# Optimization experiments

Measured on AMD Instinct MI355X. Metric: run time of the kernel, lower is better.

The kernel has to match this reference:

```python
import jax, jax.numpy as jnp
import numpy as np

H = 16          # num heads
KV_LORA = 512   # absorbed v dim
ROPE = 64       # qk_rope_head_dim
QK = KV_LORA + ROPE  # 576 absorbed qk dim
EPS = 1e-6


def rms_norm(x, w):
    xf = x.astype(jnp.float32)
    var = jnp.mean(xf * xf, axis=-1, keepdims=True)
    return (w * (xf * jax.lax.rsqrt(var + EPS))).astype(x.dtype)


def rotate_half(x):
    x1, x2 = jnp.split(x, 2, axis=-1)
    return jnp.concatenate([-x2, x1], axis=-1)


def apply_rope(x, cos, sin):
    # x: [B,S,H,ROPE]; cos/sin: [B,S,ROPE] -> broadcast over head dim
    c = cos[:, :, None, :]
    s = sin[:, :, None, :]
    return x * c + rotate_half(x) * s


def setup_inputs() -> dict:
    key = jax.random.key(0)
    ks = jax.random.split(key, 10)
    B, S, D = 1, 2048, 2048
    Q_LORA, TOPK = 1536, 512
    hidden_states = jax.random.normal(ks[0], (B, S, D), jnp.float32)
    cos = jax.random.uniform(ks[1], (B, S, ROPE), jnp.float32)
    sin = jax.random.uniform(ks[2], (B, S, ROPE), jnp.float32)
    topk = jax.random.randint(ks[3], (B, S, TOPK), 0, S)
    # guarantee the diagonal is selected so no softmax row is fully masked
    topk = topk.at[:, :, 0].set(jnp.arange(S)[None, :])
    sc = lambda f_in: 1.0 / np.sqrt(f_in)
    w_q_a = jax.random.normal(ks[4], (Q_LORA, D), jnp.float32) * sc(D)
    w_q_a_ln = jnp.ones((Q_LORA,), jnp.float32)
    w_q_b = jax.random.normal(ks[5], (H * QK, Q_LORA), jnp.float32) * sc(Q_LORA)
    w_kv_a = jax.random.normal(ks[6], (QK, D), jnp.float32) * sc(D)
    w_kv_a_ln = jnp.ones((KV_LORA,), jnp.float32)
    w_o = jax.random.normal(ks[7], (D, H * KV_LORA), jnp.float32) * sc(H * KV_LORA)
    return {"hidden_states": hidden_states, "cos": cos, "sin": sin,
            "topk_indices": topk, "w_q_a": w_q_a, "w_q_a_ln": w_q_a_ln,
            "w_q_b": w_q_b, "w_kv_a": w_kv_a, "w_kv_a_ln": w_kv_a_ln, "w_o": w_o}


def reference(hidden_states, cos, sin, topk_indices, w_q_a, w_q_a_ln, w_q_b,
              w_kv_a, w_kv_a_ln, w_o):
    B, S, D = hidden_states.shape
    # ---- Q path (low-rank + absorbed kv_b nope) ----
    q_resid = rms_norm(hidden_states @ w_q_a.T, w_q_a_ln)        # [B,S,1536]
    q = (q_resid @ w_q_b.T).reshape(B, S, H, QK)                  # [B,S,H,576]
    q_nope, q_pe = q[..., :KV_LORA], q[..., KV_LORA:]
    q_pe = apply_rope(q_pe, cos, sin)
    q = jnp.concatenate([q_nope, q_pe], axis=-1)                  # [B,S,H,576]
    # ---- shared latent KV (MQA over 576-d cache entry) ----
    ckv = hidden_states @ w_kv_a.T                                # [B,S,576]
    k_c = rms_norm(ckv[..., :KV_LORA], w_kv_a_ln)
    k_pe = apply_rope(ckv[..., KV_LORA:][:, :, None, :], cos, sin)[:, :, 0, :]
    kv = jnp.concatenate([k_c, k_pe], axis=-1)                    # [B,S,576]
    v = kv[..., :KV_LORA]                                         # [B,S,512]
    # ---- DSA sparse + causal mask ----
    allowed = jnp.zeros((B, S, S), bool)
    bi = jnp.arange(B)[:, None, None]
    si = jnp.arange(S)[None, :, None]
    allowed = allowed.at[bi, si, topk_indices].set(True)          # scatter topk
    causal = jnp.tril(jnp.ones((S, S), bool))[None]
    mask = jnp.where(allowed & causal, 0.0, -jnp.inf)[:, None]    # [B,1,S,S]
    # ---- attention ----
    scaling = QK ** (-0.5)
    scores = jnp.einsum('bshd,btd->bhst', q, kv) * scaling + mask
    probs = jax.nn.softmax(scores.astype(jnp.float32), axis=-1).astype(q.dtype)
    attn = jnp.einsum('bhst,btd->bshd', probs, v)                 # [B,S,H,512]
    out = attn.reshape(B, S, H * KV_LORA) @ w_o.T                 # [B,S,D]
    return out
```

## Files before the change

kernel.cpp:

```cpp
#include <hip/hip_runtime.h>
#include <hip/hip_bf16.h>
#include <cstdint>

#define S_LEN   2048
#define DMODEL  2048
#define HHEADS  16
#define KVLORA  512
#define ROPE_D  64
#define QKD     576
#define QLORA   1536
#define TOPK    512
#define HQK     (HHEADS * QKD)
#define HKV     (HHEADS * KVLORA)
#define NKV_PAD 640

typedef __attribute__((ext_vector_type(4))) float f4v;
typedef __attribute__((ext_vector_type(8))) short short8;
typedef __attribute__((ext_vector_type(2))) unsigned int u32x2;
typedef __attribute__((ext_vector_type(4))) unsigned int u32x4;

__device__ __forceinline__ ushort f2bf(float f) {
  uint32_t u = __float_as_uint(f);
  uint32_t r = (u + 0x7fffu + ((u >> 16) & 1u)) >> 16;
  return (ushort)r;
}
__device__ __forceinline__ float bf2f(ushort u) {
  return __uint_as_float(((uint32_t)u) << 16);
}

__device__ __forceinline__ void gload_lds16(const ushort* g, ushort* l) {
  __builtin_amdgcn_global_load_lds(
      (const __attribute__((address_space(1))) unsigned int*)(uintptr_t)g,
      (__attribute__((address_space(3))) unsigned int*)(uintptr_t)l,
      16, 0, 0);
}

__global__ __launch_bounds__(256)
void gemm_bf16_nt(const ushort* __restrict__ A, const ushort* __restrict__ B,
                  float* __restrict__ C, int M, int N, int K) {
  __shared__ ushort As[128 * 32];
  __shared__ ushort Bs[128 * 32];
  const int tid = threadIdx.x;
  const int lane = tid & 63;
  const int w = tid >> 6;
  const int wr = w >> 1, wc = w & 1;
  const int bm = blockIdx.y * 128, bn = blockIdx.x * 128;

  f4v acc[4][4];
#pragma unroll
  for (int m = 0; m < 4; ++m)
#pragma unroll
    for (int n = 0; n < 4; ++n) acc[m][n] = (f4v){0.f, 0.f, 0.f, 0.f};

  const int ar0 = w * 32;
  const int srow = lane >> 2;
  const int scol = (lane & 3) * 8;
  const int koff = (lane >> 4) * 8;
  const int fr = lane & 15;

  for (int k0 = 0; k0 < K; k0 += 32) {
    __syncthreads();
    gload_lds16(A + (size_t)(bm + ar0 + srow) * K + k0 + scol, &As[ar0 * 32]);
    gload_lds16(A + (size_t)(bm + ar0 + 16 + srow) * K + k0 + scol, &As[(ar0 + 16) * 32]);
    gload_lds16(B + (size_t)(bn + ar0 + srow) * K + k0 + scol, &Bs[ar0 * 32]);
    gload_lds16(B + (size_t)(bn + ar0 + 16 + srow) * K + k0 + scol, &Bs[(ar0 + 16) * 32]);
    __syncthreads();

    short8 a[4], b[4];
#pragma unroll
    for (int m = 0; m < 4; ++m)
      a[m] = *(const short8*)&As[(wr * 64 + m * 16 + fr) * 32 + koff];
#pragma unroll
    for (int n = 0; n < 4; ++n)
      b[n] = *(const short8*)&Bs[(wc * 64 + n * 16 + fr) * 32 + koff];
#pragma unroll
    for (int m = 0; m < 4; ++m)
#pragma unroll
      for (int n = 0; n < 4; ++n)
        acc[m][n] = __builtin_amdgcn_mfma_f32_16x16x32_bf16(a[m], b[n], acc[m][n], 0, 0, 0);
  }

  const int crow0 = bm + wr * 64 + (lane >> 4) * 4;
  const int ccol0 = bn + wc * 64 + (lane & 15);
#pragma unroll
  for (int m = 0; m < 4; ++m)
#pragma unroll
    for (int n = 0; n < 4; ++n)
#pragma unroll
      for (int r = 0; r < 4; ++r)
        C[(size_t)(crow0 + m * 16 + r) * N + ccol0 + n * 16] = acc[m][n][r];
}

__global__ __launch_bounds__(256)
void gemm_bf16_nt_bf16out(const ushort* __restrict__ A, const ushort* __restrict__ B,
                          ushort* __restrict__ C, int M, int N, int K) {
  __shared__ ushort As[128 * 32];
  __shared__ ushort Bs[128 * 32];
  const int tid = threadIdx.x;
  const int lane = tid & 63;
  const int w = tid >> 6;
  const int wr = w >> 1, wc = w & 1;
  const int bm = blockIdx.y * 128, bn = blockIdx.x * 128;

  f4v acc[4][4];
#pragma unroll
  for (int m = 0; m < 4; ++m)
#pragma unroll
    for (int n = 0; n < 4; ++n) acc[m][n] = (f4v){0.f, 0.f, 0.f, 0.f};

  const int ar0 = w * 32;
  const int srow = lane >> 2;
  const int scol = (lane & 3) * 8;
  const int koff = (lane >> 4) * 8;
  const int fr = lane & 15;

  for (int k0 = 0; k0 < K; k0 += 32) {
    __syncthreads();
    gload_lds16(A + (size_t)(bm + ar0 + srow) * K + k0 + scol, &As[ar0 * 32]);
    gload_lds16(A + (size_t)(bm + ar0 + 16 + srow) * K + k0 + scol, &As[(ar0 + 16) * 32]);
    gload_lds16(B + (size_t)(bn + ar0 + srow) * K + k0 + scol, &Bs[ar0 * 32]);
    gload_lds16(B + (size_t)(bn + ar0 + 16 + srow) * K + k0 + scol, &Bs[(ar0 + 16) * 32]);
    __syncthreads();

    short8 a[4], b[4];
#pragma unroll
    for (int m = 0; m < 4; ++m)
      a[m] = *(const short8*)&As[(wr * 64 + m * 16 + fr) * 32 + koff];
#pragma unroll
    for (int n = 0; n < 4; ++n)
      b[n] = *(const short8*)&Bs[(wc * 64 + n * 16 + fr) * 32 + koff];
#pragma unroll
    for (int m = 0; m < 4; ++m)
#pragma unroll
      for (int n = 0; n < 4; ++n)
        acc[m][n] = __builtin_amdgcn_mfma_f32_16x16x32_bf16(a[m], b[n], acc[m][n], 0, 0, 0);
  }

  const int crow0 = bm + wr * 64 + (lane >> 4) * 4;
  const int ccol0 = bn + wc * 64 + (lane & 15);
#pragma unroll
  for (int m = 0; m < 4; ++m)
#pragma unroll
    for (int n = 0; n < 4; ++n)
#pragma unroll
      for (int r = 0; r < 4; ++r)
        C[(size_t)(crow0 + m * 16 + r) * N + ccol0 + n * 16] = f2bf(acc[m][n][r]);
}

__global__ __launch_bounds__(256)
void cast_bf16(const float* __restrict__ in, ushort* __restrict__ out, int n8) {
  int i = blockIdx.x * 256 + threadIdx.x;
  if (i >= n8) return;
  float4 v0 = ((const float4*)in)[i * 2];
  float4 v1 = ((const float4*)in)[i * 2 + 1];
  short8 r;
  r[0] = f2bf(v0.x); r[1] = f2bf(v0.y); r[2] = f2bf(v0.z); r[3] = f2bf(v0.w);
  r[4] = f2bf(v1.x); r[5] = f2bf(v1.y); r[6] = f2bf(v1.z); r[7] = f2bf(v1.w);
  ((short8*)out)[i] = r;
}

__global__ __launch_bounds__(256)
void cast_pad_bf16(const float* __restrict__ in, ushort* __restrict__ out,
                   int rows_in, int cols, int n8) {
  int i = blockIdx.x * 256 + threadIdx.x;
  if (i >= n8) return;
  int row = (i * 8) / cols;
  short8 r = (short8){0, 0, 0, 0, 0, 0, 0, 0};
  if (row < rows_in) {
    float4 v0 = ((const float4*)in)[i * 2];
    float4 v1 = ((const float4*)in)[i * 2 + 1];
    r[0] = f2bf(v0.x); r[1] = f2bf(v0.y); r[2] = f2bf(v0.z); r[3] = f2bf(v0.w);
    r[4] = f2bf(v1.x); r[5] = f2bf(v1.y); r[6] = f2bf(v1.z); r[7] = f2bf(v1.w);
  }
  ((short8*)out)[i] = r;
}

__global__ __launch_bounds__(256)
void rmsnorm_bf16(const float* __restrict__ x, const float* __restrict__ w,
                  ushort* __restrict__ y, int n, float inv_n) {
  const int row = blockIdx.x;
  const float* p = x + (size_t)row * n;
  ushort* yp = y + (size_t)row * n;
  const int tid = threadIdx.x;
  const int n4 = n / 4;
  float ss = 0.f;
  for (int i = tid; i < n4; i += 256) {
    float4 v = ((const float4*)p)[i];
    ss += v.x * v.x + v.y * v.y + v.z * v.z + v.w * v.w;
  }
#pragma unroll
  for (int d = 32; d >= 1; d >>= 1) ss += __shfl_xor(ss, d);
  __shared__ float wsum[4];
  if ((tid & 63) == 0) wsum[tid >> 6] = ss;
  __syncthreads();
  float tot = wsum[0] + wsum[1] + wsum[2] + wsum[3];
  float inv = rsqrtf(tot * inv_n + 1e-6f);
  for (int i = tid; i < n4; i += 256) {
    float4 v = ((const float4*)p)[i];
    float4 g = ((const float4*)w)[i];
    ushort4 o;
    o.x = f2bf(g.x * v.x * inv); o.y = f2bf(g.y * v.y * inv);
    o.z = f2bf(g.z * v.z * inv); o.w = f2bf(g.w * v.w * inv);
    ((ushort4*)yp)[i] = o;
  }
}

__global__ __launch_bounds__(256)
void rope_scale(ushort* __restrict__ q, const float* __restrict__ cs,
                const float* __restrict__ sn) {
  const int s = blockIdx.x;
  const int tid = threadIdx.x;
  __shared__ float c_s[64], s_s[64];
  if (tid < 64) { c_s[tid] = cs[s * 64 + tid]; s_s[tid] = sn[s * 64 + tid]; }
  __syncthreads();
  const float SC = 0.041666666666666664f;
  ushort* qrow = q + (size_t)s * HQK;
  for (int i = tid; i < 1024; i += 256) {
    int hh = i >> 6, c = i & 63;
    ushort* p = qrow + hh * QKD + c * 8;
    short8 v = *(short8*)p;
#pragma unroll
    for (int e = 0; e < 8; ++e) v[e] = (short)f2bf(bf2f((ushort)v[e]) * SC);
    *(short8*)p = v;
  }
  for (int i = tid; i < HHEADS * 32; i += 256) {
    int hh = i >> 5, r = i & 31;
    ushort* bp = qrow + hh * QKD + KVLORA;
    float x1 = bf2f(bp[r]), x2 = bf2f(bp[r + 32]);
    bp[r]      = f2bf((x1 * c_s[r] - x2 * s_s[r]) * SC);
    bp[r + 32] = f2bf((x2 * c_s[r + 32] + x1 * s_s[r + 32]) * SC);
  }
}

__global__ __launch_bounds__(64)
void kv_build_bf(const float* __restrict__ ckv, const float* __restrict__ lnw,
                 const float* __restrict__ cs, const float* __restrict__ sn,
                 ushort* __restrict__ kvbf) {
  const int s = blockIdx.x;
  const int lane = threadIdx.x;
  const float* row = ckv + (size_t)s * NKV_PAD;
  float4 a = ((const float4*)row)[lane * 2];
  float4 b = ((const float4*)row)[lane * 2 + 1];
  float ss = a.x * a.x + a.y * a.y + a.z * a.z + a.w * a.w +
             b.x * b.x + b.y * b.y + b.z * b.z + b.w * b.w;
#pragma unroll
  for (int d = 32; d >= 1; d >>= 1) ss += __shfl_xor(ss, d);
  float inv = rsqrtf(ss * (1.f / KVLORA) + 1e-6f);
  float4 wa = ((const float4*)lnw)[lane * 2];
  float4 wb = ((const float4*)lnw)[lane * 2 + 1];
  ushort* orow = kvbf + (size_t)s * QKD;
  short8 o;
  o[0] = f2bf(a.x * wa.x * inv); o[1] = f2bf(a.y * wa.y * inv);
  o[2] = f2bf(a.z * wa.z * inv); o[3] = f2bf(a.w * wa.w * inv);
  o[4] = f2bf(b.x * wb.x * inv); o[5] = f2bf(b.y * wb.y * inv);
  o[6] = f2bf(b.z * wb.z * inv); o[7] = f2bf(b.w * wb.w * inv);
  *(short8*)(orow + lane * 8) = o;
  float x = row[KVLORA + lane];
  int partner = (lane < 32) ? lane + 32 : lane - 32;
  float other = row[KVLORA + partner];
  float rot = (lane < 32) ? -other : other;
  orow[KVLORA + lane] = f2bf(x * cs[s * 64 + lane] + rot * sn[s * 64 + lane]);
}

__global__ __launch_bounds__(256)
void attn_mfma(const ushort* __restrict__ qbf, const ushort* __restrict__ kvbf,
               const int* __restrict__ topk, ushort* __restrict__ attn_out) {
  const int s = blockIdx.x;
  const int tid = threadIdx.x;
  const int lane = tid & 63;
  const int w = tid >> 6;
  const int g = lane >> 4;
  const int h = lane & 15;

  __shared__ unsigned int msk[64];
  __shared__ int list[544];
  __shared__ int nk_s;
  __shared__ float wred[4][16];
  __shared__ float denom_lds[16];
  __shared__ ushort P_lds[16][520];
  __shared__ ushort VT[32 * 32 * 16];

  if (tid < 64) msk[tid] = 0u;
  {
    uint* pz = (uint*)&P_lds[0][0];
    for (int i = tid; i < 16 * 260; i += 256) pz[i] = 0u;
  }
  __syncthreads();
  for (int i = tid; i < TOPK; i += 256) {
    int t = topk[(size_t)s * TOPK + i];
    if (t <= s) atomicOr(&msk[t >> 5], 1u << (t & 31));
  }
  __syncthreads();

  if (w == 0) {
    unsigned int b = msk[lane];
    int cnt = __popc(b);
    int incl = cnt;
#pragma unroll
    for (int d = 1; d < 64; d <<= 1) {
      int o = __shfl_up(incl, d);
      if (lane >= d) incl += o;
    }
    if (lane == 63) nk_s = incl;
    int pos = incl - cnt;
    while (b) {
      int bit = __ffs(b) - 1;
      list[pos++] = (lane << 5) + bit;
      b &= b - 1;
    }
    int nkv = __shfl(incl, 63);
    for (int i = nkv + lane; i < 544; i += 64) list[i] = s;
  }

  short8 qf[18];
  const ushort* qrow = qbf + (size_t)s * HQK + h * QKD;
#pragma unroll
  for (int kk = 0; kk < 18; ++kk)
    qf[kk] = *(const short8*)(qrow + kk * 32 + g * 8);

  __syncthreads();
  const int nk = nk_s;
  const int nt16 = (nk + 15) >> 4;
  const int nkc = (nk + 31) >> 5;

  float sreg[8][4];
#pragma unroll
  for (int t2 = 0; t2 < 4; ++t2) {
    const int mtA = w + 8 * t2;
    const int mtB = mtA + 4;
    if (mtA >= nt16) break;
    const bool hasB = (mtB < nt16);
    const ushort* rA = kvbf + (size_t)list[mtA * 16 + h] * QKD;
    const ushort* rB = kvbf + (size_t)list[(hasB ? mtB : mtA) * 16 + h] * QKD;
    f4v aA = (f4v){0.f, 0.f, 0.f, 0.f};
    f4v aB = (f4v){0.f, 0.f, 0.f, 0.f};
#pragma unroll 6
    for (int kk = 0; kk < 18; ++kk) {
      short8 kfA = *(const short8*)(rA + kk * 32 + g * 8);
      short8 kfB = *(const short8*)(rB + kk * 32 + g * 8);
      aA = __builtin_amdgcn_mfma_f32_16x16x32_bf16(kfA, qf[kk], aA, 0, 0, 0);
      aB = __builtin_amdgcn_mfma_f32_16x16x32_bf16(kfB, qf[kk], aB, 0, 0, 0);
    }
#pragma unroll
    for (int r = 0; r < 4; ++r) {
      sreg[2 * t2][r] = aA[r];
      sreg[2 * t2 + 1][r] = aB[r];
    }
  }

  float mloc = -3e38f;
#pragma unroll
  for (int ti = 0; ti < 8; ++ti) {
    int keyb = 16 * (w + 4 * ti) + 4 * g;
#pragma unroll
    for (int r = 0; r < 4; ++r) {
      if (keyb + r >= nk) sreg[ti][r] = -3e38f;
      mloc = fmaxf(mloc, sreg[ti][r]);
    }
  }
  mloc = fmaxf(mloc, __shfl_xor(mloc, 16));
  mloc = fmaxf(mloc, __shfl_xor(mloc, 32));
  if (g == 0) wred[w][h] = mloc;
  __syncthreads();
  float mg = fmaxf(fmaxf(wred[0][h], wred[1][h]), fmaxf(wred[2][h], wred[3][h]));
  float psum = 0.f;
#pragma unroll
  for (int ti = 0; ti < 8; ++ti)
#pragma unroll
    for (int r = 0; r < 4; ++r) {
      float p = __expf(sreg[ti][r] - mg);
      sreg[ti][r] = p;
      psum += p;
    }
  psum += __shfl_xor(psum, 16);
  psum += __shfl_xor(psum, 32);
  __syncthreads();
  if (g == 0) wred[w][h] = psum;
  __syncthreads();
  float tot = wred[0][h] + wred[1][h] + wred[2][h] + wred[3][h];
  if (w == 0 && g == 0) denom_lds[h] = 1.0f / tot;

#pragma unroll
  for (int ti = 0; ti < 8; ++ti) {
    int mt = w + 4 * ti;
    if (mt >= nt16) break;
    uint lo = (uint)f2bf(sreg[ti][0]) | ((uint)f2bf(sreg[ti][1]) << 16);
    uint hi = (uint)f2bf(sreg[ti][2]) | ((uint)f2bf(sreg[ti][3]) << 16);
    uint* dst = (uint*)&P_lds[h][16 * mt + 4 * g];
    dst[0] = lo;
    dst[1] = hi;
  }

  f4v oacc[8];
#pragma unroll
  for (int j = 0; j < 8; ++j) oacc[j] = (f4v){0.f, 0.f, 0.f, 0.f};

  const uint vt_base = (uint)(size_t)(&VT[0]);

  for (int kc = 0; kc < nkc; ++kc) {
    __syncthreads();
#pragma unroll
    for (int ii = 0; ii < 8; ++ii) {
      int i = tid + ii * 256;
      int key = i >> 6, c = i & 63;
      const ushort* src = kvbf + (size_t)list[kc * 32 + key] * QKD + c * 8;
      short8 v = *(const short8*)src;
      *(short8*)&VT[(((c >> 1) * 32) + key) * 16 + (c & 1) * 8] = v;
    }
    __syncthreads();

    short8 pa = *(const short8*)&P_lds[h][kc * 32 + g * 8];
    u32x2 b0[8], b1[8];
#pragma unroll
    for (int j = 0; j < 8; ++j) {
      uint addr = vt_base + (uint)((w * 8 + j) * 1024 + g * 256 + h * 8);
      asm volatile("ds_read_b64_tr_b16 %0, %1 offset:0" : "=v"(b0[j]) : "v"(addr));
      asm volatile("ds_read_b64_tr_b16 %0, %1 offset:128" : "=v"(b1[j]) : "v"(addr));
    }
    asm volatile("s_waitcnt lgkmcnt(0)" ::: "memory");
    __builtin_amdgcn_sched_barrier(0);
#pragma unroll
    for (int j = 0; j < 8; ++j) {
      union { u32x4 u; short8 sv; } bb;
      bb.u = (u32x4){b0[j][0], b0[j][1], b1[j][0], b1[j][1]};
      oacc[j] = __builtin_amdgcn_mfma_f32_16x16x32_bf16(pa, bb.sv, oacc[j], 0, 0, 0);
    }
  }

  float rd[4];
#pragma unroll
  for (int r = 0; r < 4; ++r) rd[r] = denom_lds[4 * g + r];
  ushort* orow = attn_out + (size_t)s * HKV;
#pragma unroll
  for (int j = 0; j < 8; ++j) {
    int dcol = (w * 8 + j) * 16 + h;
#pragma unroll
    for (int r = 0; r < 4; ++r)
      orow[(size_t)(4 * g + r) * KVLORA + dcol] = f2bf(oacc[j][r] * rd[r]);
  }
}

extern "C" void kernel_launch(void* const* d_in, const int* in_sizes, int n_in,
                              void* d_out, int out_size, void* d_ws, size_t ws_size,
                              hipStream_t stream) {
  const float* hidden   = (const float*)d_in[0];
  const float* cosp     = (const float*)d_in[1];
  const float* sinp     = (const float*)d_in[2];
  const int*   topk     = (const int*)d_in[3];
  const float* w_q_a    = (const float*)d_in[4];
  const float* w_q_a_ln = (const float*)d_in[5];
  const float* w_q_b    = (const float*)d_in[6];
  const float* w_kv_a   = (const float*)d_in[7];
  const float* w_kv_ln  = (const float*)d_in[8];
  const float* w_o      = (const float*)d_in[9];
  float* out = (float*)d_out;

  char* base = (char*)d_ws;
  ushort* hid_bf  = (ushort*)(base + 0);
  ushort* wqa_bf  = (ushort*)(base + 8388608);
  float*  qa      = (float*) (base + 14680064);
  ushort* qa_bf   = (ushort*)(base + 27262976);
  ushort* attn_bf = (ushort*)(base + 0);
  ushort* wqb_bf  = (ushort*)(base + 33554432);
  ushort* wkv_bf  = (ushort*)(base + 61865984);
  ushort* wo_bf   = (ushort*)(base + 64487424);
  ushort* qbuf_bf = (ushort*)(base + 98041856);
  float*  ckv     = (float*) (base + 135790592);
  ushort* kv_bf   = (ushort*)(base + 141033472);

  cast_bf16<<<(S_LEN * DMODEL / 8 + 255) / 256, 256, 0, stream>>>(hidden, hid_bf, S_LEN * DMODEL / 8);
  cast_bf16<<<(QLORA * DMODEL / 8 + 255) / 256, 256, 0, stream>>>(w_q_a, wqa_bf, QLORA * DMODEL / 8);
  cast_bf16<<<(HQK * QLORA / 8 + 255) / 256, 256, 0, stream>>>(w_q_b, wqb_bf, HQK * QLORA / 8);
  cast_pad_bf16<<<(NKV_PAD * DMODEL / 8 + 255) / 256, 256, 0, stream>>>(w_kv_a, wkv_bf, QKD, DMODEL, NKV_PAD * DMODEL / 8);
  cast_bf16<<<(DMODEL * HKV / 8 + 255) / 256, 256, 0, stream>>>(w_o, wo_bf, DMODEL * HKV / 8);

  gemm_bf16_nt<<<dim3(QLORA / 128, S_LEN / 128), 256, 0, stream>>>(
      hid_bf, wqa_bf, qa, S_LEN, QLORA, DMODEL);
  rmsnorm_bf16<<<S_LEN, 256, 0, stream>>>(qa, w_q_a_ln, qa_bf, QLORA, 1.f / QLORA);

  gemm_bf16_nt_bf16out<<<dim3(HQK / 128, S_LEN / 128), 256, 0, stream>>>(
      qa_bf, wqb_bf, qbuf_bf, S_LEN, HQK, QLORA);
  rope_scale<<<S_LEN, 256, 0, stream>>>(qbuf_bf, cosp, sinp);

  gemm_bf16_nt<<<dim3(NKV_PAD / 128, S_LEN / 128), 256, 0, stream>>>(
      hid_bf, wkv_bf, ckv, S_LEN, NKV_PAD, DMODEL);
  kv_build_bf<<<S_LEN, 64, 0, stream>>>(ckv, w_kv_ln, cosp, sinp, kv_bf);

  attn_mfma<<<S_LEN, 256, 0, stream>>>(qbuf_bf, kv_bf, topk, attn_bf);

  gemm_bf16_nt<<<dim3(DMODEL / 128, S_LEN / 128), 256, 0, stream>>>(
      attn_bf, wo_bf, out, S_LEN, DMODEL, HKV);
}
```

Before: 755.8 us.

## Template GEMM with double-buffered LDS staging and per-call tile shapes

Replaces the two GEMM kernels with one templated kernel. It double-buffers the LDS tiles so the global_load_lds for the next K-slice is issued before the MFMAs of the current one, leaving one barrier per iteration instead of two. Each projection also gets its own tile shape: 64x128 for the q_a and output GEMMs and 64x64 for the small kv_a GEMM, which raises the workgroup count on the 256-CU device. The costs are doubled LDS footprint and smaller tiles that reuse less data. The async LDS loads are not explicitly waited on before the barrier, so correctness depends on the compiler inserting vmcnt waits.

```diff
diff --git a/kernel.cpp b/kernel.cpp
--- a/kernel.cpp
+++ b/kernel.cpp
@@ -35,116 +35,83 @@
       16, 0, 0);
 }
 
-__global__ __launch_bounds__(256)
-void gemm_bf16_nt(const ushort* __restrict__ A, const ushort* __restrict__ B,
-                  float* __restrict__ C, int M, int N, int K) {
-  __shared__ ushort As[128 * 32];
-  __shared__ ushort Bs[128 * 32];
+template<int BM, int BN, int WGM, int WGN, bool BF16OUT>
+__global__ __launch_bounds__(256)
+void gemm_nt_t(const ushort* __restrict__ A, const ushort* __restrict__ B,
+               void* __restrict__ Cv, int M, int N, int K) {
+  constexpr int MR = BM / (WGM * 16);
+  constexpr int NR = BN / (WGN * 16);
+  __shared__ ushort As[2][BM * 32];
+  __shared__ ushort Bs[2][BN * 32];
   const int tid = threadIdx.x;
   const int lane = tid & 63;
   const int w = tid >> 6;
-  const int wr = w >> 1, wc = w & 1;
-  const int bm = blockIdx.y * 128, bn = blockIdx.x * 128;
-
-  f4v acc[4][4];
-#pragma unroll
-  for (int m = 0; m < 4; ++m)
-#pragma unroll
-    for (int n = 0; n < 4; ++n) acc[m][n] = (f4v){0.f, 0.f, 0.f, 0.f};
-
-  const int ar0 = w * 32;
-  const int srow = lane >> 2;
+  const int wr = w / WGN, wc = w % WGN;
+  const int bm = blockIdx.y * BM, bn = blockIdx.x * BN;
+  const int srow16 = w * 16 + (lane >> 2);
   const int scol = (lane & 3) * 8;
   const int koff = (lane >> 4) * 8;
   const int fr = lane & 15;
 
-  for (int k0 = 0; k0 < K; k0 += 32) {
+  f4v acc[MR][NR];
+#pragma unroll
+  for (int m = 0; m < MR; ++m)
+#pragma unroll
+    for (int n = 0; n < NR; ++n) acc[m][n] = (f4v){0.f, 0.f, 0.f, 0.f};
+
+  auto STAGE = [&](int buf, int k0) {
+#pragma unroll
+    for (int r0 = 0; r0 < BM; r0 += 64)
+      gload_lds16(A + (size_t)(bm + r0 + srow16) * K + k0 + scol,
+                  &As[buf][(r0 + w * 16) * 32]);
+#pragma unroll
+    for (int r0 = 0; r0 < BN; r0 += 64)
+      gload_lds16(B + (size_t)(bn + r0 + srow16) * K + k0 + scol,
+                  &Bs[buf][(r0 + w * 16) * 32]);
+  };
+
+  const int nt = K / 32;
+  int cur = 0;
+  STAGE(0, 0);
+  for (int t = 0; t < nt; ++t) {
     __syncthreads();
-    gload_lds16(A + (size_t)(bm + ar0 + srow) * K + k0 + scol, &As[ar0 * 32]);
-    gload_lds16(A + (size_t)(bm + ar0 + 16 + srow) * K + k0 + scol, &As[(ar0 + 16) * 32]);
-    gload_lds16(B + (size_t)(bn + ar0 + srow) * K + k0 + scol, &Bs[ar0 * 32]);
-    gload_lds16(B + (size_t)(bn + ar0 + 16 + srow) * K + k0 + scol, &Bs[(ar0 + 16) * 32]);
-    __syncthreads();
-
-    short8 a[4], b[4];
-#pragma unroll
-    for (int m = 0; m < 4; ++m)
-      a[m] = *(const short8*)&As[(wr * 64 + m * 16 + fr) * 32 + koff];
-#pragma unroll
-    for (int n = 0; n < 4; ++n)
-      b[n] = *(const short8*)&Bs[(wc * 64 + n * 16 + fr) * 32 + koff];
-#pragma unroll
-    for (int m = 0; m < 4; ++m)
-#pragma unroll
-      for (int n = 0; n < 4; ++n)
+    if (t + 1 < nt) STAGE(cur ^ 1, (t + 1) * 32);
+    short8 a[MR], b[NR];
+#pragma unroll
+    for (int m = 0; m < MR; ++m)
+      a[m] = *(const short8*)&As[cur][(wr * MR * 16 + m * 16 + fr) * 32 + koff];
+#pragma unroll
+    for (int n = 0; n < NR; ++n)
+      b[n] = *(const short8*)&Bs[cur][(wc * NR * 16 + n * 16 + fr) * 32 + koff];
+#pragma unroll
+    for (int m = 0; m < MR; ++m)
+#pragma unroll
+      for (int n = 0; n < NR; ++n)
         acc[m][n] = __builtin_amdgcn_mfma_f32_16x16x32_bf16(a[m], b[n], acc[m][n], 0, 0, 0);
-  }
-
-  const int crow0 = bm + wr * 64 + (lane >> 4) * 4;
-  const int ccol0 = bn + wc * 64 + (lane & 15);
-#pragma unroll
-  for (int m = 0; m < 4; ++m)
-#pragma unroll
-    for (int n = 0; n < 4; ++n)
-#pragma unroll
-      for (int r = 0; r < 4; ++r)
-        C[(size_t)(crow0 + m * 16 + r) * N + ccol0 + n * 16] = acc[m][n][r];
-}
-
-__global__ __launch_bounds__(256)
-void gemm_bf16_nt_bf16out(const ushort* __restrict__ A, const ushort* __restrict__ B,
-                          ushort* __restrict__ C, int M, int N, int K) {
-  __shared__ ushort As[128 * 32];
-  __shared__ ushort Bs[128 * 32];
-  const int tid = threadIdx.x;
-  const int lane = tid & 63;
-  const int w = tid >> 6;
-  const int wr = w >> 1, wc = w & 1;
-  const int bm = blockIdx.y * 128, bn = blockIdx.x * 128;
-
-  f4v acc[4][4];
-#pragma unroll
-  for (int m = 0; m < 4; ++m)
-#pragma unroll
-    for (int n = 0; n < 4; ++n) acc[m][n] = (f4v){0.f, 0.f, 0.f, 0.f};
-
-  const int ar0 = w * 32;
-  const int srow = lane >> 2;
-  const int scol = (lane & 3) * 8;
-  const int koff = (lane >> 4) * 8;
-  const int fr = lane & 15;
-
-  for (int k0 = 0; k0 < K; k0 += 32) {
-    __syncthreads();
-    gload_lds16(A + (size_t)(bm + ar0 + srow) * K + k0 + scol, &As[ar0 * 32]);
-    gload_lds16(A + (size_t)(bm + ar0 + 16 + srow) * K + k0 + scol, &As[(ar0 + 16) * 32]);
-    gload_lds16(B + (size_t)(bn + ar0 + srow) * K + k0 + scol, &Bs[ar0 * 32]);
-    gload_lds16(B + (size_t)(bn + ar0 + 16 + srow) * K + k0 + scol, &Bs[(ar0 + 16) * 32]);
-    __syncthreads();
-
-    short8 a[4], b[4];
-#pragma unroll
-    for (int m = 0; m < 4; ++m)
-      a[m] = *(const short8*)&As[(wr * 64 + m * 16 + fr) * 32 + koff];
-#pragma unroll
-    for (int n = 0; n < 4; ++n)
-      b[n] = *(const short8*)&Bs[(wc * 64 + n * 16 + fr) * 32 + koff];
-#pragma unroll
-    for (int m = 0; m < 4; ++m)
-#pragma unroll
-      for (int n = 0; n < 4; ++n)
-        acc[m][n] = __builtin_amdgcn_mfma_f32_16x16x32_bf16(a[m], b[n], acc[m][n], 0, 0, 0);
-  }
-
-  const int crow0 = bm + wr * 64 + (lane >> 4) * 4;
-  const int ccol0 = bn + wc * 64 + (lane & 15);
-#pragma unroll
-  for (int m = 0; m < 4; ++m)
-#pragma unroll
-    for (int n = 0; n < 4; ++n)
-#pragma unroll
-      for (int r = 0; r < 4; ++r)
-        C[(size_t)(crow0 + m * 16 + r) * N + ccol0 + n * 16] = f2bf(acc[m][n][r]);
+    cur ^= 1;
+  }
+
+  const int crow0 = bm + wr * MR * 16 + (lane >> 4) * 4;
+  const int ccol0 = bn + wc * NR * 16 + fr;
+  if constexpr (BF16OUT) {
+    ushort* C = (ushort*)Cv;
+#pragma unroll
+    for (int m = 0; m < MR; ++m)
+#pragma unroll
+      for (int n = 0; n < NR; ++n)
+#pragma unroll
+        for (int r = 0; r < 4; ++r)
+          C[(size_t)(crow0 + m * 16 + r) * N + ccol0 + n * 16] = f2bf(acc[m][n][r]);
+  } else {
+    float* C = (float*)Cv;
+#pragma unroll
+    for (int m = 0; m < MR; ++m)
+#pragma unroll
+      for (int n = 0; n < NR; ++n)
+#pragma unroll
+        for (int r = 0; r < 4; ++r)
+          C[(size_t)(crow0 + m * 16 + r) * N + ccol0 + n * 16] = acc[m][n][r];
+  }
 }
 
 __global__ __launch_bounds__(256)
@@ -474,20 +441,20 @@
   cast_pad_bf16<<<(NKV_PAD * DMODEL / 8 + 255) / 256, 256, 0, stream>>>(w_kv_a, wkv_bf, QKD, DMODEL, NKV_PAD * DMODEL / 8);
   cast_bf16<<<(DMODEL * HKV / 8 + 255) / 256, 256, 0, stream>>>(w_o, wo_bf, DMODEL * HKV / 8);
 
-  gemm_bf16_nt<<<dim3(QLORA / 128, S_LEN / 128), 256, 0, stream>>>(
+  gemm_nt_t<64, 128, 1, 4, false><<<dim3(QLORA / 128, S_LEN / 64), 256, 0, stream>>>(
       hid_bf, wqa_bf, qa, S_LEN, QLORA, DMODEL);
   rmsnorm_bf16<<<S_LEN, 256, 0, stream>>>(qa, w_q_a_ln, qa_bf, QLORA, 1.f / QLORA);
 
-  gemm_bf16_nt_bf16out<<<dim3(HQK / 128, S_LEN / 128), 256, 0, stream>>>(
+  gemm_nt_t<128, 128, 2, 2, true><<<dim3(HQK / 128, S_LEN / 128), 256, 0, stream>>>(
       qa_bf, wqb_bf, qbuf_bf, S_LEN, HQK, QLORA);
   rope_scale<<<S_LEN, 256, 0, stream>>>(qbuf_bf, cosp, sinp);
 
-  gemm_bf16_nt<<<dim3(NKV_PAD / 128, S_LEN / 128), 256, 0, stream>>>(
+  gemm_nt_t<64, 64, 2, 2, false><<<dim3(NKV_PAD / 64, S_LEN / 64), 256, 0, stream>>>(
       hid_bf, wkv_bf, ckv, S_LEN, NKV_PAD, DMODEL);
   kv_build_bf<<<S_LEN, 64, 0, stream>>>(ckv, w_kv_ln, cosp, sinp, kv_bf);
 
   attn_mfma<<<S_LEN, 256, 0, stream>>>(qbuf_bf, kv_bf, topk, attn_bf);
 
-  gemm_bf16_nt<<<dim3(DMODEL / 128, S_LEN / 128), 256, 0, stream>>>(
+  gemm_nt_t<64, 128, 1, 4, false><<<dim3(DMODEL / 128, S_LEN / 64), 256, 0, stream>>>(
       attn_bf, wo_bf, out, S_LEN, DMODEL, HKV);
 }
```

New measurement: 635.1 us. -16.0%, faster.
